# Performance work log

Measured on AMD Instinct MI355X. Metric: run time of the kernel, lower is better.

## Reference

```python
import jax, jax.numpy as jnp
import numpy as np

N = 65536          # nodes
K = 12             # graph_k
CHUNK = 1024       # graph_knn_chunk (capped at 1024 in source)
WIDTH = 256        # mlp width
GWIDTH = 192       # graph width
DEPTH = 7          # mlp depth
GLAYERS = 4        # graph layers
COND = 64          # cond_dim
NUM_FF = 8         # fourier num per sigma
SIGMAS = (1.0, 10.0, 50.0)
SKIPS = (3, 6)     # residual skips
OUT_SCALE = 0.01
FF_DIM = 2 * len(SIGMAS) * NUM_FF  # 48 (sin+cos per sigma band)


def fourier_feats(x, B):
    # x: (N,3), B: (S,3,NUM_FF) -> (N, 2*S*NUM_FF)
    proj = jnp.einsum('nd,sdm->nsm', x, B).reshape(x.shape[0], -1)
    return jnp.concatenate([jnp.sin(proj), jnp.cos(proj)], axis=-1)


def knn_graph(x):
    # chunked exact kNN: mirrors _build_knn_graph (chunked cdist + top-k)
    x_sq = jnp.sum(x * x, axis=1)  # (N,)
    n = x.shape[0]
    col_ids = jnp.arange(n)

    def chunk_fn(start):
        rows = start + jnp.arange(CHUNK)
        xc = x[rows]                                   # (C,3)
        d = x_sq[rows][:, None] + x_sq[None, :] - 2.0 * (xc @ x.T)  # (C,N)
        d = jnp.maximum(d, 0.0)
        d = d + jnp.where(rows[:, None] == col_ids[None, :], 1e9, 0.0)  # exclude self
        _, idx = jax.lax.top_k(-d, K)                  # k smallest distances
        return idx

    idx = jax.lax.map(chunk_fn, jnp.arange(0, n, CHUNK))  # (n/C, C, K)
    return idx.reshape(n, K)


def setup_inputs() -> dict:
    key = jax.random.key(0)
    ks = jax.random.split(key, 16)
    g = lambda k, shape, fan: jax.random.normal(k, shape, jnp.float32) / np.sqrt(fan)
    sig = jnp.asarray(SIGMAS, jnp.float32)[:, None, None]
    return {
        'x': jax.random.normal(ks[0], (N, 3), jnp.float32),
        'cond': jax.random.normal(ks[1], (COND,), jnp.float32),
        'B': jax.random.normal(ks[2], (len(SIGMAS), 3, NUM_FF), jnp.float32) * sig,
        'W_in': g(ks[3], (FF_DIM, WIDTH), FF_DIM),
        'b_in': jnp.zeros((WIDTH,), jnp.float32),
        'Wg_in': g(ks[4], (FF_DIM, GWIDTH), FF_DIM),
        'bg_in': jnp.zeros((GWIDTH,), jnp.float32),
        'Ws': g(ks[5], (GLAYERS, GWIDTH, GWIDTH), GWIDTH),
        'Wn': g(ks[6], (GLAYERS, GWIDTH, GWIDTH), GWIDTH),
        'bg': jnp.zeros((GLAYERS, GWIDTH), jnp.float32),
        'Wg_out': g(ks[7], (GWIDTH, WIDTH), GWIDTH),
        'W': g(ks[8], (DEPTH, WIDTH, WIDTH), WIDTH),
        'bmlp': jnp.zeros((DEPTH, WIDTH), jnp.float32),
        'Wf_g': g(ks[9], (DEPTH, COND, WIDTH), COND),
        'bf_g': jnp.zeros((DEPTH, WIDTH), jnp.float32),
        'Wf_b': g(ks[10], (DEPTH, COND, WIDTH), COND),
        'bf_b': jnp.zeros((DEPTH, WIDTH), jnp.float32),
        'W_out': g(ks[11], (WIDTH, 3), WIDTH),
        'b_out': jnp.zeros((3,), jnp.float32),
    }


def reference(x, cond, B, W_in, b_in, Wg_in, bg_in, Ws, Wn, bg, Wg_out,
              W, bmlp, Wf_g, bf_g, Wf_b, bf_b, W_out, b_out):
    act = jax.nn.silu
    knn_idx = knn_graph(x)                     # (N,K) graph structure
    ff = fourier_feats(x, B)                   # (N,48)
    h0 = act(ff @ W_in + b_in)                 # (N,256) coordinate embedding

    # graph message-passing branch (row-normalized 1/K adjacency == neighbor mean)
    gfeat = act(ff @ Wg_in + bg_in)            # (N,192)
    for l in range(GLAYERS):
        agg = jnp.mean(gfeat[knn_idx], axis=1)  # sparse spmm: gather + mean
        gfeat = act(gfeat @ Ws[l] + agg @ Wn[l] + bg[l])

    h = h0 + gfeat @ Wg_out                    # inject graph context

    # FiLM-conditioned residual MLP trunk
    for l in range(DEPTH):
        gamma = cond @ Wf_g[l] + bf_g[l]       # (256,)
        beta = cond @ Wf_b[l] + bf_b[l]
        h = act((h @ W[l] + bmlp[l]) * (1.0 + gamma) + beta)
        if (l + 1) in SKIPS:
            h = h + h0

    return (h @ W_out + b_out) * OUT_SCALE     # (N,3) displacement
```

## Files before the change

kernel.cpp:

```cpp
#include <hip/hip_runtime.h>
#include <math.h>

#define NN      65536
#define KNN     12
#define WIDTH   256
#define GW      192
#define DEPTH   7
#define GLAYERS 4
#define FF      48

#define GC    192
#define GC3   7077888
#define GLO   (-6.0f)
#define GCW   0.0625f
#define GINV  16.0f

#define GS     128
#define GS3    2097152
#define GSINV  10.666666667f
#define CS2    0.09375f

#define QL    16

typedef __attribute__((ext_vector_type(8))) _Float16 half8;
typedef __attribute__((ext_vector_type(4))) _Float16 half4;
typedef __attribute__((ext_vector_type(4))) float    f4;

__device__ __forceinline__ float silu_f(float v) { return v / (1.0f + expf(-v)); }

#define KSWAP(A,B,IA,IB) do { if (B < A) { float _t=A; A=B; B=_t; int _u=IA; IA=IB; IB=_u; } } while(0)
#define KINSERT(DV,IV) do { b11=(DV); j11=(IV); \
    KSWAP(b10,b11,j10,j11); KSWAP(b9,b10,j9,j10); KSWAP(b8,b9,j8,j9); \
    KSWAP(b7,b8,j7,j8);  KSWAP(b6,b7,j6,j7);  KSWAP(b5,b6,j5,j6); \
    KSWAP(b4,b5,j4,j5);  KSWAP(b3,b4,j3,j4);  KSWAP(b2,b3,j2,j3); \
    KSWAP(b1,b2,j1,j2);  KSWAP(b0,b1,j0,j1); } while(0)

__device__ __forceinline__ int cell_of(float v) {
    int c = (int)floorf((v - GLO) * GINV);
    return min(max(c, 0), GC-1);
}

__device__ __forceinline__ int cell2(float v) {
    int c = (int)floorf((v - GLO) * GSINV);
    return min(max(c, 0), GS-1);
}

__global__ __launch_bounds__(256) void zero_both_kernel(int* __restrict__ cnt,
                                                        int* __restrict__ cnt2) {
    int g = blockIdx.x*256 + threadIdx.x;
    if (g < GC3/4) *(int4*)&cnt[g*4] = make_int4(0,0,0,0);
    else           *(int4*)&cnt2[(g - GC3/4)*4] = make_int4(0,0,0,0);
}

__global__ __launch_bounds__(256) void prep_hist_kernel(const float* __restrict__ x,
                                                        float4* __restrict__ xw,
                                                        int* __restrict__ cnt,
                                                        int* __restrict__ cnt2) {
    int i = blockIdx.x*256 + threadIdx.x;
    float a = x[3*i], b = x[3*i+1], c = x[3*i+2];
    xw[i] = make_float4(a, b, c, a*a + b*b + c*c);
    atomicAdd(&cnt[(cell_of(c)*GC + cell_of(b))*GC + cell_of(a)], 1);
    atomicAdd(&cnt2[(cell2(c)*GS + cell2(b))*GS + cell2(a)], 1);
}

__global__ __launch_bounds__(256) void satx_kernel(int* __restrict__ S) {
    int zy = blockIdx.x*256 + threadIdx.x;
    int base = zy * GC, run = 0;
    for (int i = 0; i < GC; ++i) { run += S[base+i]; S[base+i] = run; }
}
__global__ __launch_bounds__(256) void saty_kernel(int* __restrict__ S) {
    int t = blockIdx.x*256 + threadIdx.x;
    int z = t / GC, xx = t % GC, run = 0;
    for (int y = 0; y < GC; ++y) { int idx = (z*GC + y)*GC + xx; run += S[idx]; S[idx] = run; }
}
__global__ __launch_bounds__(256) void satz_kernel(int* __restrict__ S) {
    int t = blockIdx.x*256 + threadIdx.x;
    int y = t / GC, xx = t % GC, run = 0;
    for (int z = 0; z < GC; ++z) { int idx = (z*GC + y)*GC + xx; run += S[idx]; S[idx] = run; }
}

__device__ __forceinline__ int satv(const int* __restrict__ S, int xx, int y, int z) {
    if (xx < 0 || y < 0 || z < 0) return 0;
    return S[(z*GC + y)*GC + xx];
}

__global__ __launch_bounds__(256) void seed_kernel(const float4* __restrict__ xw,
                                                   const int* __restrict__ S,
                                                   float* __restrict__ seed) {
    int q = blockIdx.x*256 + threadIdx.x;
    float4 me = xw[q];
    int cx = cell_of(me.x), cy = cell_of(me.y), cz = cell_of(me.z);
    for (int R = 1; R < GC; ++R) {
        int x0 = max(cx-R, 0), x1 = min(cx+R, GC-1);
        int y0 = max(cy-R, 0), y1 = min(cy+R, GC-1);
        int z0 = max(cz-R, 0), z1 = min(cz+R, GC-1);
        int c = satv(S,x1,y1,z1) - satv(S,x0-1,y1,z1) - satv(S,x1,y0-1,z1) - satv(S,x1,y1,z0-1)
              + satv(S,x0-1,y0-1,z1) + satv(S,x0-1,y1,z0-1) + satv(S,x1,y0-1,z0-1)
              - satv(S,x0-1,y0-1,z0-1);
        if (c >= KNN + 1) {
            float dx = fmaxf(me.x - (GLO + x0*GCW), (GLO + (x1+1)*GCW) - me.x);
            float dy = fmaxf(me.y - (GLO + y0*GCW), (GLO + (y1+1)*GCW) - me.y);
            float dz = fmaxf(me.z - (GLO + z0*GCW), (GLO + (z1+1)*GCW) - me.z);
            seed[q] = (dx*dx + dy*dy + dz*dz) * 1.00002f + 1e-6f;
            return;
        }
    }
    seed[q] = 3e38f;
}

__global__ __launch_bounds__(256) void scan1_kernel(const int* __restrict__ cnt,
                                                    int* __restrict__ bsum) {
    __shared__ int red[256];
    const int t = threadIdx.x;
    int4 v = ((const int4*)cnt)[blockIdx.x*256 + t];
    red[t] = v.x + v.y + v.z + v.w;
    __syncthreads();
    for (int off = 128; off > 0; off >>= 1) {
        if (t < off) red[t] += red[t + off];
        __syncthreads();
    }
    if (t == 0) bsum[blockIdx.x] = red[0];
}

__global__ __launch_bounds__(256) void scan2_kernel(int* __restrict__ bsum) {
    __shared__ int red[256];
    const int t = threadIdx.x;
    int v[8]; int s = 0;
#pragma unroll
    for (int i = 0; i < 8; ++i) { v[i] = bsum[t*8 + i]; s += v[i]; }
    red[t] = s;
    __syncthreads();
    for (int off = 1; off < 256; off <<= 1) {
        int x = (t >= off) ? red[t - off] : 0;
        __syncthreads();
        red[t] += x;
        __syncthreads();
    }
    int run = red[t] - s;
#pragma unroll
    for (int i = 0; i < 8; ++i) { int c = v[i]; bsum[t*8 + i] = run; run += c; }
}

__global__ __launch_bounds__(256) void scan3_kernel(int* __restrict__ cnt,
                                                    const int* __restrict__ bsum) {
    __shared__ int red[256];
    const int t = threadIdx.x;
    int4 v = ((const int4*)cnt)[blockIdx.x*256 + t];
    int s = v.x + v.y + v.z + v.w;
    red[t] = s;
    __syncthreads();
    for (int off = 1; off < 256; off <<= 1) {
        int x = (t >= off) ? red[t - off] : 0;
        __syncthreads();
        red[t] += x;
        __syncthreads();
    }
    int run = bsum[blockIdx.x] + red[t] - s;
    int4 o;
    o.x = run; run += v.x;
    o.y = run; run += v.y;
    o.z = run; run += v.z;
    o.w = run;
    ((int4*)cnt)[blockIdx.x*256 + t] = o;
}

__global__ __launch_bounds__(256) void scatter_kernel(const float4* __restrict__ xw,
                                                      int* __restrict__ cstart,
                                                      float4* __restrict__ sxw,
                                                      int* __restrict__ sid) {
    int i = blockIdx.x*256 + threadIdx.x;
    float4 p = xw[i];
    int cid = (cell2(p.z)*GS + cell2(p.y))*GS + cell2(p.x);
    int pos = atomicAdd(&cstart[cid], 1);
    sxw[pos] = p;
    sid[pos] = i;
}

#define MROUND(M) do { \
    float pb0=__shfl_xor(b0,M), pb1=__shfl_xor(b1,M), pb2=__shfl_xor(b2,M), \
          pb3=__shfl_xor(b3,M), pb4=__shfl_xor(b4,M), pb5=__shfl_xor(b5,M), \
          pb6=__shfl_xor(b6,M), pb7=__shfl_xor(b7,M), pb8=__shfl_xor(b8,M), \
          pb9=__shfl_xor(b9,M), pb10=__shfl_xor(b10,M), pb11=__shfl_xor(b11,M); \
    int  pj0=__shfl_xor(j0,M), pj1=__shfl_xor(j1,M), pj2=__shfl_xor(j2,M), \
         pj3=__shfl_xor(j3,M), pj4=__shfl_xor(j4,M), pj5=__shfl_xor(j5,M), \
         pj6=__shfl_xor(j6,M), pj7=__shfl_xor(j7,M), pj8=__shfl_xor(j8,M), \
         pj9=__shfl_xor(j9,M), pj10=__shfl_xor(j10,M), pj11=__shfl_xor(j11,M); \
    if (pb0  < b11) KINSERT(pb0, pj0);   if (pb1  < b11) KINSERT(pb1, pj1); \
    if (pb2  < b11) KINSERT(pb2, pj2);   if (pb3  < b11) KINSERT(pb3, pj3); \
    if (pb4  < b11) KINSERT(pb4, pj4);   if (pb5  < b11) KINSERT(pb5, pj5); \
    if (pb6  < b11) KINSERT(pb6, pj6);   if (pb7  < b11) KINSERT(pb7, pj7); \
    if (pb8  < b11) KINSERT(pb8, pj8);   if (pb9  < b11) KINSERT(pb9, pj9); \
    if (pb10 < b11) KINSERT(pb10, pj10); if (pb11 < b11) KINSERT(pb11, pj11); \
} while(0)

__global__ __launch_bounds__(256) void knn_direct_kernel(const float4* __restrict__ sxw,
                                                         const int* __restrict__ sid,
                                                         const int* __restrict__ cend,
                                                         const float* __restrict__ seed,
                                                         unsigned short* __restrict__ knn_idx) {
    const int gtid = blockIdx.x*256 + threadIdx.x;
    const int p   = gtid >> 4;
    const int sub = gtid & (QL-1);
    const float4 me = sxw[p];
    const float qsq = me.w;
    const float rr = seed[sid[p]] + 1e-3f;
    const float r = sqrtf(rr);
    const int y0 = cell2(me.y - r), y1 = cell2(me.y + r);
    const int z0 = cell2(me.z - r), z1 = cell2(me.z + r);
    const int Wy = y1 - y0 + 1;
    const int NZ = z1 - z0 + 1;

    float b0=3e38f,b1=3e38f,b2=3e38f,b3=3e38f,b4=3e38f,b5=3e38f,
          b6=3e38f,b7=3e38f,b8=3e38f,b9=3e38f,b10=3e38f,b11=3e38f;
    int   j0=-1,j1=-1,j2=-1,j3=-1,j4=-1,j5=-1,j6=-1,j7=-1,j8=-1,j9=-1,j10=-1,j11=-1;

    int zi = sub / Wy;
    int yi = sub - zi*Wy;
    const int zstep = QL / Wy;
    const int ystep = QL - zstep*Wy;

    auto rowspan = [&](int zi_, int yi_, int& t0, int& te) {
        t0 = 0; te = 0;
        if (zi_ < NZ) {
            int zz = z0 + zi_, yy = y0 + yi_;
            float ylo = (yy == 0)    ? -1e30f : GLO + yy*CS2;
            float yhi = (yy == GS-1) ?  1e30f : GLO + (yy+1)*CS2;
            float dy = fmaxf(0.0f, fmaxf(ylo - me.y, me.y - yhi));
            float zlo = (zz == 0)    ? -1e30f : GLO + zz*CS2;
            float zhi = (zz == GS-1) ?  1e30f : GLO + (zz+1)*CS2;
            float dz = fmaxf(0.0f, fmaxf(zlo - me.z, me.z - zhi));
            float rbl = fminf(rr, b11 * 1.00002f + 1e-6f);
            float rem = rbl - dy*dy - dz*dz;
            if (rem > 0.0f) {
                float xr = sqrtf(rem);
                int xl = cell2(me.x - xr), xh = cell2(me.x + xr);
                int crow = (zz*GS + yy)*GS;
                int c0 = crow + xl;
                t0 = c0 ? cend[c0-1] : 0;
                te = cend[crow + xh];
            }
        }
    };

    int t0c, tec;
    rowspan(zi, yi, t0c, tec);
    while (zi < NZ) {
        int ziN = zi + zstep, yiN = yi + ystep;
        if (yiN >= Wy) { yiN -= Wy; ++ziN; }
        int t0n, ten;
        rowspan(ziN, yiN, t0n, ten);
        for (int t = t0c; t < tec; ++t) {
            float4 c = sxw[t];
            float dot = me.x*c.x + me.y*c.y + me.z*c.z;
            float d = fmaf(-2.0f, dot, qsq + c.w);
            d = fmaxf(d, 0.0f);
            if (d < rr && d < b11 && t != p) KINSERT(d, t);
        }
        zi = ziN; yi = yiN; t0c = t0n; tec = ten;
    }
    MROUND(1); MROUND(2); MROUND(4); MROUND(8);
    if (sub == 0) {
        knn_idx[p*KNN+0]=(unsigned short)j0;  knn_idx[p*KNN+1]=(unsigned short)j1;
        knn_idx[p*KNN+2]=(unsigned short)j2;  knn_idx[p*KNN+3]=(unsigned short)j3;
        knn_idx[p*KNN+4]=(unsigned short)j4;  knn_idx[p*KNN+5]=(unsigned short)j5;
        knn_idx[p*KNN+6]=(unsigned short)j6;  knn_idx[p*KNN+7]=(unsigned short)j7;
        knn_idx[p*KNN+8]=(unsigned short)j8;  knn_idx[p*KNN+9]=(unsigned short)j9;
        knn_idx[p*KNN+10]=(unsigned short)j10; knn_idx[p*KNN+11]=(unsigned short)j11;
    }
}

__global__ __launch_bounds__(256) void convert_Wt_kernel(const float* __restrict__ W,
                                                         _Float16* __restrict__ Wt) {
    int e = blockIdx.x*256 + threadIdx.x;
    int l = e >> 16, r = e & 65535;
    int n = r >> 8, k = r & 255;
    Wt[(size_t)l*65536 + n*256 + k] = (_Float16)W[(size_t)l*65536 + k*256 + n];
}

__global__ __launch_bounds__(256) void convert_Bg_kernel(const float* __restrict__ Ws,
                                                         const float* __restrict__ Wn,
                                                         _Float16* __restrict__ Bg) {
    int e = blockIdx.x*256 + threadIdx.x;
    int l = e / 73728, r = e % 73728;
    int n = r / 384, k = r % 384;
    float v = (k < 192) ? Ws[(size_t)l*36864 + k*192 + n]
                        : Wn[(size_t)l*36864 + (k-192)*192 + n];
    Bg[(size_t)l*73728 + (size_t)n*384 + k] = (_Float16)v;
}

__global__ __launch_bounds__(256) void convert_Wgo_kernel(const float* __restrict__ Wg_out,
                                                          _Float16* __restrict__ Wgo) {
    int e = blockIdx.x*256 + threadIdx.x;
    int n = e / 192, k = e % 192;
    Wgo[e] = (_Float16)Wg_out[k*256 + n];
}

__global__ __launch_bounds__(256) void convert_Win_kernel(const float* __restrict__ W_in,
                                                          const float* __restrict__ Wg_in,
                                                          _Float16* __restrict__ WinT,
                                                          _Float16* __restrict__ WginT) {
    int e = blockIdx.x*256 + threadIdx.x;
    if (e < 16384) {
        int n = e >> 6, k = e & 63;
        WinT[e] = (_Float16)(k < FF ? W_in[k*WIDTH + n] : 0.0f);
    } else {
        int e2 = e - 16384;
        int n = e2 >> 6, k = e2 & 63;
        WginT[e2] = (_Float16)(k < FF ? Wg_in[k*GW + n] : 0.0f);
    }
}

__global__ __launch_bounds__(256) void ff_kernel(const float4* __restrict__ sxw,
                                                 const float* __restrict__ Bf,
                                                 _Float16* __restrict__ fft) {
    const int n = blockIdx.x * 256 + threadIdx.x;
    const float4 pos = sxw[n];
    const float x0 = pos.x, x1 = pos.y, x2 = pos.z;
    _Float16 v[64];
#pragma unroll
    for (int sm = 0; sm < 24; ++sm) {
        int s = sm >> 3, m = sm & 7;
        float p = x0*Bf[s*24 + m] + x1*Bf[s*24 + 8 + m] + x2*Bf[s*24 + 16 + m];
        float sv, cv; sincosf(p, &sv, &cv);
        v[sm] = (_Float16)sv; v[24 + sm] = (_Float16)cv;
    }
#pragma unroll
    for (int k = 48; k < 64; ++k) v[k] = (_Float16)0.0f;
#pragma unroll
    for (int k8 = 0; k8 < 8; ++k8)
        *(half8*)&fft[(size_t)n*64 + k8*8] = *(half8*)&v[k8*8];
}

__global__ __launch_bounds__(192) void gather_mean_kernel(const _Float16* __restrict__ g,
                                                          const unsigned short* __restrict__ idx,
                                                          _Float16* __restrict__ agg) {
    __shared__ unsigned short nb[8][KNN];
    const int t = threadIdx.x;
    const int nb8 = blockIdx.x * 8;
    if (t < 96) { int nn = t / 12, kk = t - nn*12; nb[nn][kk] = idx[(nb8+nn)*KNN + kk]; }
    __syncthreads();
    const int nloc = t / 24, c8 = t % 24;
    float acc[8] = {0,0,0,0,0,0,0,0};
#pragma unroll
    for (int k = 0; k < KNN; ++k) {
        half8 v = *(const half8*)&g[(size_t)nb[nloc][k]*GW + c8*8];
#pragma unroll
        for (int u = 0; u < 8; ++u) acc[u] += (float)v[u];
    }
    half8 o;
#pragma unroll
    for (int u = 0; u < 8; ++u) o[u] = (_Float16)(acc[u] * (1.0f/12.0f));
    *(half8*)&agg[(size_t)(nb8 + nloc)*GW + c8*8] = o;
}

__global__ __launch_bounds__(256) void film_kernel(const float* __restrict__ cond,
                                                   const float* __restrict__ Wf_g,
                                                   const float* __restrict__ bf_g,
                                                   const float* __restrict__ Wf_b,
                                                   const float* __restrict__ bf_b,
                                                   float* __restrict__ film) {
    const int l = blockIdx.x, j = threadIdx.x;
    float g = bf_g[l*WIDTH + j], b = bf_b[l*WIDTH + j];
    for (int c = 0; c < 64; ++c) {
        float cv = cond[c];
        g = fmaf(cv, Wf_g[(size_t)(l*64 + c)*WIDTH + j], g);
        b = fmaf(cv, Wf_b[(size_t)(l*64 + c)*WIDTH + j], b);
    }
    film[l*2*WIDTH + j]         = 1.0f + g;
    film[l*2*WIDTH + WIDTH + j] = b;
}

template<int EPI>
__global__ __launch_bounds__(256) void gemm_mfma(
    const _Float16* __restrict__ A1, const _Float16* __restrict__ A2,
    const _Float16* __restrict__ Bt, int K1, int Ktot, int NC,
    const float* __restrict__ bias, const float* __restrict__ film,
    const _Float16* __restrict__ h0, _Float16* __restrict__ C, int addSkip) {
    __shared__ _Float16 As[128*40];
    __shared__ _Float16 Bs[64*40];
    const int tid = threadIdx.x;
    const int bm = blockIdx.x * 128, bn = blockIdx.y * 64;
    const int wid = tid >> 6, lane = tid & 63;
    const int wm = (wid & 1) * 64, wn = (wid >> 1) * 32;
    const int m16 = lane & 15, kq = lane >> 4;
    const int ar = tid >> 1, ah = tid & 1;
    const int br = tid >> 2, bq = tid & 3;
    f4 acc[4][2];
#pragma unroll
    for (int i = 0; i < 4; ++i)
#pragma unroll
        for (int j = 0; j < 2; ++j) acc[i][j] = (f4){0.f, 0.f, 0.f, 0.f};

    for (int kc = 0; kc < Ktot; kc += 32) {
        const _Float16* Asrc; int kl, ldA;
        if (kc < K1) { Asrc = A1; kl = kc;      ldA = K1; }
        else         { Asrc = A2; kl = kc - K1; ldA = Ktot - K1; }
        {
            const float4* src = (const float4*)&Asrc[(size_t)(bm + ar)*ldA + kl + ah*16];
            *(float4*)&As[ar*40 + ah*16]     = src[0];
            *(float4*)&As[ar*40 + ah*16 + 8] = src[1];
        }
        *(float4*)&Bs[br*40 + bq*8] = *(const float4*)&Bt[(size_t)(bn + br)*Ktot + kc + bq*8];
        __syncthreads();
        half8 af[4], bf[2];
#pragma unroll
        for (int mt = 0; mt < 4; ++mt) af[mt] = *(half8*)&As[(wm + mt*16 + m16)*40 + kq*8];
#pragma unroll
        for (int nt = 0; nt < 2; ++nt) bf[nt] = *(half8*)&Bs[(wn + nt*16 + m16)*40 + kq*8];
#pragma unroll
        for (int mt = 0; mt < 4; ++mt)
#pragma unroll
            for (int nt = 0; nt < 2; ++nt)
                acc[mt][nt] = __builtin_amdgcn_mfma_f32_16x16x32_f16(af[mt], bf[nt], acc[mt][nt], 0, 0, 0);
        __syncthreads();
    }

#pragma unroll
    for (int mt = 0; mt < 4; ++mt) {
#pragma unroll
        for (int nt = 0; nt < 2; ++nt) {
            int col = bn + wn + nt*16 + m16;
#pragma unroll
            for (int r = 0; r < 4; ++r) {
                int row = bm + wm + mt*16 + kq*4 + r;
                float v = acc[mt][nt][r];
                if (EPI == 0) {
                    v = silu_f(v + bias[col]);
                } else if (EPI == 1) {
                    v = fmaf(v + bias[col], film[col], film[NC + col]);
                    v = silu_f(v);
                    if (addSkip) v += (float)h0[(size_t)row*NC + col];
                } else {
                    v += (float)h0[(size_t)row*NC + col];
                }
                C[(size_t)row*NC + col] = (_Float16)v;
            }
        }
    }
}

__global__ __launch_bounds__(256) void out_kernel(const _Float16* __restrict__ h,
                                                  const int* __restrict__ sid,
                                                  const float* __restrict__ W_out,
                                                  const float* __restrict__ b_out,
                                                  float* __restrict__ out) {
    const int n = blockIdx.x * 256 + threadIdx.x;
    float a0 = 0.f, a1 = 0.f, a2 = 0.f;
#pragma unroll 4
    for (int k8 = 0; k8 < WIDTH/8; ++k8) {
        half8 v = *(const half8*)&h[(size_t)n*WIDTH + k8*8];
#pragma unroll
        for (int u = 0; u < 8; ++u) {
            float f = (float)v[u]; int k = k8*8 + u;
            a0 = fmaf(f, W_out[k*3+0], a0);
            a1 = fmaf(f, W_out[k*3+1], a1);
            a2 = fmaf(f, W_out[k*3+2], a2);
        }
    }
    const int o = sid[n];
    out[o*3+0] = (a0 + b_out[0]) * 0.01f;
    out[o*3+1] = (a1 + b_out[1]) * 0.01f;
    out[o*3+2] = (a2 + b_out[2]) * 0.01f;
}

extern "C" void kernel_launch(void* const* d_in, const int* in_sizes, int n_in,
                              void* d_out, int out_size, void* d_ws, size_t ws_size,
                              hipStream_t stream) {
    const float* x      = (const float*)d_in[0];
    const float* cond   = (const float*)d_in[1];
    const float* Bf     = (const float*)d_in[2];
    const float* W_in   = (const float*)d_in[3];
    const float* b_in   = (const float*)d_in[4];
    const float* Wg_in  = (const float*)d_in[5];
    const float* bg_in  = (const float*)d_in[6];
    const float* Ws     = (const float*)d_in[7];
    const float* Wn     = (const float*)d_in[8];
    const float* bg     = (const float*)d_in[9];
    const float* Wg_out = (const float*)d_in[10];
    const float* W      = (const float*)d_in[11];
    const float* bmlp   = (const float*)d_in[12];
    const float* Wf_g   = (const float*)d_in[13];
    const float* bf_g   = (const float*)d_in[14];
    const float* Wf_b   = (const float*)d_in[15];
    const float* bf_b   = (const float*)d_in[16];
    const float* W_out  = (const float*)d_in[17];
    const float* b_out  = (const float*)d_in[18];
    float* out = (float*)d_out;

    char* ws = (char*)d_ws;
    unsigned short* knn_idx = (unsigned short*)(ws + 0);
    int*       sid     = (int*)      (ws + 1572864);
    float4*    xw      = (float4*)   (ws + 3145728);
    _Float16*  WinT    = (_Float16*) (ws + 3145728);
    _Float16*  WginT   = (_Float16*) (ws + 3178496);
    float*     film    = (float*)    (ws + 4194304);
    _Float16*  Bg_t    = (_Float16*) (ws + 4210688);
    _Float16*  Wgo_t   = (_Float16*) (ws + 4800512);
    _Float16*  Wt      = (_Float16*) (ws + 4898816);
    _Float16*  h0      = (_Float16*) (ws + 5816320);
    int*       cnt     = (int*)      (ws + 5816320);
    float*     seed    = (float*)    (ws + 34127872);
    _Float16*  g_a     = (_Float16*) (ws + 39370752);
    int*       cellCnt = (int*)      (ws + 39370752);
    int*       bsum    = (int*)      (ws + 47759360);
    float4*    sxw     = (float4*)   (ws + 47767552);
    _Float16*  g_b     = (_Float16*) (ws + 64536576);
    _Float16*  agg     = (_Float16*) (ws + 89702400);
    _Float16*  hA      = (_Float16*) (ws + 114868224);
    _Float16*  hB      = (_Float16*) (ws + 148422656);
    _Float16*  fft     = (_Float16*) (ws + 148422656);

    zero_both_kernel<<<(GC3+GS3)/1024, 256, 0, stream>>>(cnt, cellCnt);
    prep_hist_kernel<<<NN/256, 256, 0, stream>>>(x, xw, cnt, cellCnt);
    satx_kernel<<<GC*GC/256, 256, 0, stream>>>(cnt);
    saty_kernel<<<GC*GC/256, 256, 0, stream>>>(cnt);
    satz_kernel<<<GC*GC/256, 256, 0, stream>>>(cnt);
    seed_kernel<<<NN/256, 256, 0, stream>>>(xw, cnt, seed);

    scan1_kernel<<<GS3/1024, 256, 0, stream>>>(cellCnt, bsum);
    scan2_kernel<<<1, 256, 0, stream>>>(bsum);
    scan3_kernel<<<GS3/1024, 256, 0, stream>>>(cellCnt, bsum);
    scatter_kernel<<<NN/256, 256, 0, stream>>>(xw, cellCnt, sxw, sid);
    knn_direct_kernel<<<NN*QL/256, 256, 0, stream>>>(sxw, sid, cellCnt, seed, knn_idx);

    film_kernel<<<DEPTH, 256, 0, stream>>>(cond, Wf_g, bf_g, Wf_b, bf_b, film);
    convert_Wt_kernel<<<DEPTH*65536/256, 256, 0, stream>>>(W, Wt);
    convert_Bg_kernel<<<GLAYERS*73728/256, 256, 0, stream>>>(Ws, Wn, Bg_t);
    convert_Wgo_kernel<<<256*192/256, 256, 0, stream>>>(Wg_out, Wgo_t);
    convert_Win_kernel<<<28672/256, 256, 0, stream>>>(W_in, Wg_in, WinT, WginT);
    ff_kernel<<<NN/256, 256, 0, stream>>>(sxw, Bf, fft);
    gemm_mfma<0><<<dim3(NN/128, WIDTH/64), 256, 0, stream>>>(
        fft, nullptr, WinT, 64, 64, WIDTH, b_in, nullptr, nullptr, h0, 0);
    gemm_mfma<0><<<dim3(NN/128, GW/64), 256, 0, stream>>>(
        fft, nullptr, WginT, 64, 64, GW, bg_in, nullptr, nullptr, g_a, 0);

    _Float16* gin = g_a; _Float16* gout = g_b;
    for (int l = 0; l < GLAYERS; ++l) {
        gather_mean_kernel<<<NN/8, 192, 0, stream>>>(gin, knn_idx, agg);
        gemm_mfma<0><<<dim3(NN/128, GW/64), 256, 0, stream>>>(
            gin, agg, Bg_t + (size_t)l*73728, GW, 2*GW, GW,
            bg + l*GW, nullptr, nullptr, gout, 0);
        _Float16* t = gin; gin = gout; gout = t;
    }
    gemm_mfma<2><<<dim3(NN/128, WIDTH/64), 256, 0, stream>>>(
        gin, nullptr, Wgo_t, GW, GW, WIDTH, nullptr, nullptr, h0, hA, 0);

    _Float16* hin = hA; _Float16* hout = hB;
    for (int l = 0; l < DEPTH; ++l) {
        int skip = (l == 2 || l == 5) ? 1 : 0;
        gemm_mfma<1><<<dim3(NN/128, WIDTH/64), 256, 0, stream>>>(
            hin, nullptr, Wt + (size_t)l*65536, WIDTH, WIDTH, WIDTH,
            bmlp + l*WIDTH, film + l*2*WIDTH, h0, hout, skip);
        _Float16* t = hin; hin = hout; hout = t;
    }
    out_kernel<<<NN/256, 256, 0, stream>>>(hin, sid, W_out, b_out, out);
}
```

Before: 1.003 ms.

## Use wave-level scan for SAT x-pass and binary search for kNN seed radius

The x-direction prefix sum of the summed-area table now gives each 192-long row to one 64-lane wavefront. It runs a shuffle-based inclusive scan over three segments, replacing one thread serially walking strided memory. The seed kernel finds the smallest box radius holding at least K+1 points by exponential doubling then binary search, instead of a linear scan of radii. This cuts uncoalesced memory traffic and serial latency, at the cost of more blocks and possibly more SAT lookups for points whose neighbours are very close.

```diff
diff --git a/kernel.cpp b/kernel.cpp
--- a/kernel.cpp
+++ b/kernel.cpp
@@ -64,10 +64,24 @@
 }
 
 __global__ __launch_bounds__(256) void satx_kernel(int* __restrict__ S) {
-    int zy = blockIdx.x*256 + threadIdx.x;
-    int base = zy * GC, run = 0;
-    for (int i = 0; i < GC; ++i) { run += S[base+i]; S[base+i] = run; }
-}
+    const int wid  = (blockIdx.x*256 + threadIdx.x) >> 6;
+    const int lane = threadIdx.x & 63;
+    const int base = wid * GC;
+    int carry = 0;
+#pragma unroll
+    for (int seg = 0; seg < 3; ++seg) {
+        int v = S[base + seg*64 + lane];
+#pragma unroll
+        for (int off = 1; off < 64; off <<= 1) {
+            int n = __shfl_up(v, off);
+            if (lane >= off) v += n;
+        }
+        v += carry;
+        S[base + seg*64 + lane] = v;
+        carry = __shfl(v, 63);
+    }
+}
+
 __global__ __launch_bounds__(256) void saty_kernel(int* __restrict__ S) {
     int t = blockIdx.x*256 + threadIdx.x;
     int z = t / GC, xx = t % GC, run = 0;
@@ -90,22 +104,37 @@
     int q = blockIdx.x*256 + threadIdx.x;
     float4 me = xw[q];
     int cx = cell_of(me.x), cy = cell_of(me.y), cz = cell_of(me.z);
-    for (int R = 1; R < GC; ++R) {
+
+    auto boxcount = [&](int R) {
         int x0 = max(cx-R, 0), x1 = min(cx+R, GC-1);
         int y0 = max(cy-R, 0), y1 = min(cy+R, GC-1);
         int z0 = max(cz-R, 0), z1 = min(cz+R, GC-1);
-        int c = satv(S,x1,y1,z1) - satv(S,x0-1,y1,z1) - satv(S,x1,y0-1,z1) - satv(S,x1,y1,z0-1)
-              + satv(S,x0-1,y0-1,z1) + satv(S,x0-1,y1,z0-1) + satv(S,x1,y0-1,z0-1)
-              - satv(S,x0-1,y0-1,z0-1);
-        if (c >= KNN + 1) {
-            float dx = fmaxf(me.x - (GLO + x0*GCW), (GLO + (x1+1)*GCW) - me.x);
-            float dy = fmaxf(me.y - (GLO + y0*GCW), (GLO + (y1+1)*GCW) - me.y);
-            float dz = fmaxf(me.z - (GLO + z0*GCW), (GLO + (z1+1)*GCW) - me.z);
-            seed[q] = (dx*dx + dy*dy + dz*dz) * 1.00002f + 1e-6f;
-            return;
-        }
-    }
-    seed[q] = 3e38f;
+        return satv(S,x1,y1,z1) - satv(S,x0-1,y1,z1) - satv(S,x1,y0-1,z1) - satv(S,x1,y1,z0-1)
+             + satv(S,x0-1,y0-1,z1) + satv(S,x0-1,y1,z0-1) + satv(S,x1,y0-1,z0-1)
+             - satv(S,x0-1,y0-1,z0-1);
+    };
+
+    int Rlo = 0, Rhi = 1;
+    int c = boxcount(1);
+    while (c < KNN + 1) {
+        if (Rhi >= GC - 1) break;
+        Rlo = Rhi;
+        Rhi = min(Rhi << 1, GC - 1);
+        c = boxcount(Rhi);
+    }
+    if (c < KNN + 1) { seed[q] = 3e38f; return; }
+    while (Rlo + 1 < Rhi) {
+        int Rm = (Rlo + Rhi) >> 1;
+        if (boxcount(Rm) >= KNN + 1) Rhi = Rm; else Rlo = Rm;
+    }
+    const int R = Rhi;
+    int x0 = max(cx-R, 0), x1 = min(cx+R, GC-1);
+    int y0 = max(cy-R, 0), y1 = min(cy+R, GC-1);
+    int z0 = max(cz-R, 0), z1 = min(cz+R, GC-1);
+    float dx = fmaxf(me.x - (GLO + x0*GCW), (GLO + (x1+1)*GCW) - me.x);
+    float dy = fmaxf(me.y - (GLO + y0*GCW), (GLO + (y1+1)*GCW) - me.y);
+    float dz = fmaxf(me.z - (GLO + z0*GCW), (GLO + (z1+1)*GCW) - me.z);
+    seed[q] = (dx*dx + dy*dy + dz*dz) * 1.00002f + 1e-6f;
 }
 
 __global__ __launch_bounds__(256) void scan1_kernel(const int* __restrict__ cnt,
@@ -512,7 +541,7 @@
 
     zero_both_kernel<<<(GC3+GS3)/1024, 256, 0, stream>>>(cnt, cellCnt);
     prep_hist_kernel<<<NN/256, 256, 0, stream>>>(x, xw, cnt, cellCnt);
-    satx_kernel<<<GC*GC/256, 256, 0, stream>>>(cnt);
+    satx_kernel<<<GC*GC/4, 256, 0, stream>>>(cnt);
     saty_kernel<<<GC*GC/256, 256, 0, stream>>>(cnt);
     satz_kernel<<<GC*GC/256, 256, 0, stream>>>(cnt);
     seed_kernel<<<NN/256, 256, 0, stream>>>(xw, cnt, seed);
```

New measurement: 987.9 us. No clear change (-1.5%).
